# Performance work log

Measured on AMD Instinct MI355X. Metric: run time of the kernel, lower is better.

## Reference

```python
import jax, jax.numpy as jnp
import numpy as np
from jax import lax

IN_FEATURES = 1024
NUM_TAGS = 128
C = NUM_TAGS + 3          # CRF adds start/stop (+1 pad slot per original code)
START_IDX = C - 2
STOP_IDX = C - 1
NEG = -10000.0


def setup_inputs() -> dict:
    key = jax.random.key(0)
    k1, k2, k3, k4 = jax.random.split(key, 4)
    B, L = 64, 512
    x = jax.random.normal(k1, (B, L, IN_FEATURES), dtype=jnp.float32)
    mask = jnp.ones((B, L), dtype=jnp.float32)
    W = jax.random.normal(k2, (C, IN_FEATURES), dtype=jnp.float32) * (1.0 / np.sqrt(IN_FEATURES))
    b = jax.random.normal(k3, (C,), dtype=jnp.float32) * 0.01
    transitions = jax.random.normal(k4, (C, C), dtype=jnp.float32)
    # transitions[i, j] = score of transitioning FROM j TO i
    transitions = transitions.at[START_IDX, :].set(NEG)   # never transition into start
    transitions = transitions.at[:, STOP_IDX].set(NEG)    # never transition out of stop
    return {"x": x, "mask": mask, "W": W, "b": b, "transitions": transitions}


def reference(x, mask, W, b, transitions):
    """CRF forward: linear projection + Viterbi decode.
    Returns (best_score [B], best_paths [B, L])."""
    feats = jnp.einsum("bld,cd->blc", x, W) + b          # [B, L, C]
    B, L, Cn = feats.shape

    init_score = jnp.full((B, Cn), NEG, dtype=feats.dtype).at[:, START_IDX].set(0.0)

    def viterbi_step(score, inp):
        feat_t, mask_t = inp                              # [B, C], [B]
        # acc[b, i, j] = score[b, j] + transitions[i, j]
        acc = score[:, None, :] + transitions[None, :, :]  # [B, C, C]
        best = jnp.max(acc, axis=-1)                      # [B, C]
        bp = jnp.argmax(acc, axis=-1).astype(jnp.int32)   # [B, C]
        m = mask_t[:, None]
        new_score = (best + feat_t) * m + score * (1.0 - m)
        return new_score, bp

    final_score, bps = lax.scan(
        viterbi_step, init_score,
        (jnp.transpose(feats, (1, 0, 2)), mask.T))        # bps: [L, B, C]

    final_score = final_score + transitions[STOP_IDX]     # [B, C]
    best_score = jnp.max(final_score, axis=-1)            # [B]
    best_tag = jnp.argmax(final_score, axis=-1).astype(jnp.int32)  # [B]

    def backtrack(tag, bp_t):
        # tag: current tag at timestep t; bp_t: [B, C] backpointers at t
        prev = jnp.take_along_axis(bp_t, tag[:, None], axis=1)[:, 0]
        return prev, tag                                  # emit tag at timestep t

    _, path = lax.scan(backtrack, best_tag, bps, reverse=True)  # path: [L, B]
    best_paths = path.T                                   # [B, L]
    return best_score, best_paths
```

## Files before the change

### kernel.cpp

```cpp
#include <hip/hip_runtime.h>

#define BB 64
#define LL 512
#define DD 1024
#define CC 131
#define CP 132
#define START_I 129
#define STOP_I 130
#define NEGV -10000.0f

__device__ __forceinline__ void lds_barrier() {
    asm volatile("s_waitcnt lgkmcnt(0)" ::: "memory");
    __builtin_amdgcn_s_barrier();
    __builtin_amdgcn_sched_barrier(0);
}

#define GM 64
#define GK 32
#define LSTR 36

__global__ __launch_bounds__(256, 2) void gemm_feats(
    const float* __restrict__ x, const float* __restrict__ W,
    const float* __restrict__ bias, float* __restrict__ feats)
{
    __shared__ float xs[GM * LSTR];
    __shared__ float ws[CP * LSTR];

    const int tid = threadIdx.x;
    const int m0 = blockIdx.x * GM;
    const int tm = tid & 15;
    const int tj = (tid >> 4) & 15;
    const bool tail = (tj < 3);
    const int tjt = (tj < 3) ? tj : 2;

    float acc[4][8];
    float acct[4];
#pragma unroll
    for (int r = 0; r < 4; ++r) {
        acct[r] = 0.f;
#pragma unroll
        for (int c = 0; c < 8; ++c) acc[r][c] = 0.f;
    }

    for (int kc = 0; kc < DD / GK; ++kc) {
        const int k0 = kc * GK;
        if (kc) __syncthreads();
#pragma unroll
        for (int q = 0; q < 2; ++q) {
            int lin = tid + q * 256;
            int m = lin >> 3, c4 = lin & 7;
            float4 v = *(const float4*)&x[(size_t)(m0 + m) * DD + k0 + c4 * 4];
            *(float4*)&xs[m * LSTR + c4 * 4] = v;
        }
#pragma unroll
        for (int q = 0; q < 5; ++q) {
            int lin = tid + q * 256;
            if (lin < CC * 8) {
                int r = lin >> 3, c4 = lin & 7;
                float4 v = *(const float4*)&W[(size_t)r * DD + k0 + c4 * 4];
                *(float4*)&ws[r * LSTR + c4 * 4] = v;
            }
        }
        __syncthreads();

#pragma unroll
        for (int k4 = 0; k4 < 8; ++k4) {
            float4 xr[4], wr[8], wt;
#pragma unroll
            for (int r = 0; r < 4; ++r)
                xr[r] = *(const float4*)&xs[(tm + 16 * r) * LSTR + k4 * 4];
#pragma unroll
            for (int c = 0; c < 8; ++c)
                wr[c] = *(const float4*)&ws[(tj + 16 * c) * LSTR + k4 * 4];
            wt = *(const float4*)&ws[(128 + tjt) * LSTR + k4 * 4];
#pragma unroll
            for (int r = 0; r < 4; ++r) {
#pragma unroll
                for (int c = 0; c < 8; ++c) {
                    acc[r][c] = fmaf(xr[r].x, wr[c].x, acc[r][c]);
                    acc[r][c] = fmaf(xr[r].y, wr[c].y, acc[r][c]);
                    acc[r][c] = fmaf(xr[r].z, wr[c].z, acc[r][c]);
                    acc[r][c] = fmaf(xr[r].w, wr[c].w, acc[r][c]);
                }
                acct[r] = fmaf(xr[r].x, wt.x, acct[r]);
                acct[r] = fmaf(xr[r].y, wt.y, acct[r]);
                acct[r] = fmaf(xr[r].z, wt.z, acct[r]);
                acct[r] = fmaf(xr[r].w, wt.w, acct[r]);
            }
        }
    }

#pragma unroll
    for (int c = 0; c < 8; ++c) {
        int j = tj + 16 * c;
        float bv = bias[j];
#pragma unroll
        for (int r = 0; r < 4; ++r)
            feats[(size_t)(m0 + tm + 16 * r) * CP + j] = acc[r][c] + bv;
    }
    if (tail) {
        int j = 128 + tj;
        float bv = bias[j];
#pragma unroll
        for (int r = 0; r < 4; ++r)
            feats[(size_t)(m0 + tm + 16 * r) * CP + j] = acct[r] + bv;
    }
}

__global__ __launch_bounds__(576, 1) void viterbi_fwd(
    const float* __restrict__ feats, const float* __restrict__ mask,
    const float* __restrict__ trans, float* __restrict__ hist)
{
    const int b = blockIdx.x;
    const int tid = threadIdx.x;
    const int w = tid >> 6, lane = tid & 63;

    int row, sub;
    bool scw;
    if (w < 8) {
        row = (w >> 2) * 64 + lane;
        sub = w & 3;
        scw = true;
    } else {
        int r = 128 + (lane >> 2);
        row = (r <= 130) ? r : 130;
        sub = lane & 3;
        scw = (lane < 12);
    }

    __shared__ float sbuf[2][160];
    __shared__ float pbuf[4][136];

    float4 T[10];
    {
        const float* tr = trans + (size_t)row * CC;
        const int base = sub * 40;
#pragma unroll
        for (int q = 0; q < 10; ++q) {
            float vx = NEGV, vy = NEGV, vz = NEGV, vw = NEGV;
            int i = base + 4 * q;
            if (i + 0 < CC) vx = tr[i + 0];
            if (i + 1 < CC) vy = tr[i + 1];
            if (i + 2 < CC) vz = tr[i + 2];
            if (i + 3 < CC) vw = tr[i + 3];
            T[q].x = vx; T[q].y = vy; T[q].z = vz; T[q].w = vw;
        }
    }

    for (int q = tid; q < 2 * 160; q += 576) {
        int bi = q / 160, idx = q - bi * 160;
        sbuf[bi][idx] = (bi == 0 && idx == START_I) ? 0.f : NEGV;
    }
    __syncthreads();

    const float* fb = feats + (size_t)b * LL * CP;
    const float* mb = mask + (size_t)b * LL;
    float* hb = hist + (size_t)b * LL * CP;

    const int k = tid;
    const bool cmb = (tid < 131);
    float s_prev = (k == START_I) ? 0.f : NEGV;
    float fv0 = 0.f, fv1 = 0.f, mv0 = 1.f, mv1 = 1.f;
    const float* fb_t = fb + 2 * CP + k;
    const float* mb_t = mb + 2;
    float* hb_k = hb + k;
    if (cmb) { fv0 = fb[k]; fv1 = fb[CP + k]; mv0 = mb[0]; mv1 = mb[1]; }

    for (int t = 0; t < LL; ++t) {
        const int rb = t & 1;

        {
            const float4* s4 = (const float4*)sbuf[rb] + sub * 10;
            float a0 = -3.0e38f, a1 = -3.0e38f, a2 = -3.0e38f, a3 = -3.0e38f;
#pragma unroll
            for (int q = 0; q < 5; ++q) {
                float4 sv = s4[q]; float4 t4 = T[q];
                a0 = fmaxf(fmaxf(sv.x + t4.x, sv.y + t4.y), a0);
                a1 = fmaxf(fmaxf(sv.z + t4.z, sv.w + t4.w), a1);
            }
#pragma unroll
            for (int q = 5; q < 10; ++q) {
                float4 sv = s4[q]; float4 t4 = T[q];
                a2 = fmaxf(fmaxf(sv.x + t4.x, sv.y + t4.y), a2);
                a3 = fmaxf(fmaxf(sv.z + t4.z, sv.w + t4.w), a3);
            }
            if (scw) pbuf[sub][row] = fmaxf(fmaxf(a0, a1), fmaxf(a2, a3));
        }

        lds_barrier();

        if (cmb) {
            float fv2 = 0.f, mv2 = 1.f;
            if (t + 2 < LL) { fv2 = *fb_t; mv2 = *mb_t; }
            fb_t += CP; ++mb_t;

            float p = fmaxf(fmaxf(pbuf[0][k], pbuf[1][k]),
                            fmaxf(pbuf[2][k], pbuf[3][k]));
            float ns = (mv0 != 0.f) ? (p + fv0) : s_prev;
            s_prev = ns;
            sbuf[rb ^ 1][k] = ns;
            *hb_k = ns;
            hb_k += CP;

            fv0 = fv1; fv1 = fv2; mv0 = mv1; mv1 = mv2;
        }

        lds_barrier();
    }
}

__global__ __launch_bounds__(256, 4) void bp_kernel(
    const float* __restrict__ hist, const float* __restrict__ trans,
    unsigned char* __restrict__ bp)
{
    const int b  = blockIdx.x / 5;
    const int jc = blockIdx.x % 5;
    const int tc = blockIdx.y;
    const int tid = threadIdx.x;
    const int j0 = jc * 32;

    __shared__ float Ts[32][136];
    __shared__ float hs[8][132];

    for (int q = 0; q < 17; ++q) {
        int lin = tid + q * 256;
        if (lin < 32 * CC) {
            int r = lin / CC, i = lin - r * CC;
            if (j0 + r < CC) Ts[r][i] = trans[(size_t)(j0 + r) * CC + i];
        }
    }
    {
        const float4* src = (const float4*)(hist + ((size_t)b * LL + tc * 8) * CP);
#pragma unroll
        for (int q = 0; q < 2; ++q) {
            int lin = tid + q * 256;
            if (lin < (8 * CP) / 4) ((float4*)hs)[lin] = src[lin];
        }
    }
    __syncthreads();

    const int jl = tid & 31;
    const int tt = tid >> 5;
    const int j = j0 + jl;
    const int t = tc * 8 + tt + 1;
    if (j >= CC || t >= LL) return;

    float best; int idx;
    {
        float4 tv = *(const float4*)&Ts[jl][128];
        float4 hv = *(const float4*)&hs[tt][128];
        best = hv.z + tv.z; idx = 130;
        float v;
        v = hv.y + tv.y; if (v >= best) { best = v; idx = 129; }
        v = hv.x + tv.x; if (v >= best) { best = v; idx = 128; }
    }
#pragma unroll
    for (int i4 = 31; i4 >= 0; --i4) {
        float4 tv = *(const float4*)&Ts[jl][i4 * 4];
        float4 hv = *(const float4*)&hs[tt][i4 * 4];
        float v;
        v = hv.w + tv.w; if (v >= best) { best = v; idx = i4 * 4 + 3; }
        v = hv.z + tv.z; if (v >= best) { best = v; idx = i4 * 4 + 2; }
        v = hv.y + tv.y; if (v >= best) { best = v; idx = i4 * 4 + 1; }
        v = hv.x + tv.x; if (v >= best) { best = v; idx = i4 * 4 + 0; }
    }
    bp[((size_t)b * LL + t) * CP + j] = (unsigned char)idx;
}

__global__ __launch_bounds__(64, 1) void viterbi_btr(
    const float* __restrict__ hist, const float* __restrict__ trans,
    const unsigned char* __restrict__ bp,
    float* __restrict__ out_score, float* __restrict__ out_path)
{
    const int b = blockIdx.x;
    const int lane = threadIdx.x;
    const float* hb = hist + ((size_t)b * LL + (LL - 1)) * CP;
    const float* ts = trans + (size_t)STOP_I * CC;

    float v0 = hb[lane] + ts[lane];
    float v1 = hb[lane + 64] + ts[lane + 64];
    float v2 = (lane < 3) ? (hb[lane + 128] + ts[lane + 128]) : -3.0e38f;

    float best = v0; int idx = lane;
    if (v1 > best) { best = v1; idx = lane + 64; }
    if (v2 > best) { best = v2; idx = lane + 128; }
#pragma unroll
    for (int off = 32; off >= 1; off >>= 1) {
        float ob = __shfl_xor(best, off, 64);
        int   oi = __shfl_xor(idx, off, 64);
        if (ob > best || (ob == best && oi < idx)) { best = ob; idx = oi; }
    }

    float* op = out_path + (size_t)b * LL;
    if (lane == 0) {
        out_score[b] = best;
        op[LL - 1] = (float)idx;
    }
    int tag = idx;

    __shared__ unsigned char buf[2][1088];
    const unsigned char* bpb = bp + (size_t)b * LL * CP;

    {
        const unsigned int* src = (const unsigned int*)(bpb + (size_t)504 * CP);
        unsigned int* dst = (unsigned int*)buf[1];
#pragma unroll
        for (int q = 0; q < 5; ++q) {
            int lin = lane + q * 64;
            if (lin < 264) dst[lin] = src[lin];
        }
    }
    lds_barrier();

    int cur = 1;
    for (int k = 63; k >= 0; --k) {
        unsigned int r0 = 0, r1 = 0, r2 = 0, r3 = 0, r4 = 0;
        if (k > 0) {
            const unsigned int* src = (const unsigned int*)(bpb + (size_t)(k - 1) * 8 * CP);
            r0 = src[lane];
            r1 = src[lane + 64];
            r2 = src[lane + 128];
            r3 = src[lane + 192];
            if (lane < 8) r4 = src[lane + 256];
        }
        const unsigned char* cb = buf[cur];
#pragma unroll
        for (int s = 7; s >= 0; --s) {
            int t = k * 8 + s;
            if (t >= 1) {
                tag = cb[s * CP + tag];
                if (lane == 0) op[t - 1] = (float)tag;
            }
        }
        if (k > 0) {
            unsigned int* dst = (unsigned int*)buf[cur ^ 1];
            dst[lane] = r0;
            dst[lane + 64] = r1;
            dst[lane + 128] = r2;
            dst[lane + 192] = r3;
            if (lane < 8) dst[lane + 256] = r4;
            lds_barrier();
        }
        cur ^= 1;
    }
}

extern "C" void kernel_launch(void* const* d_in, const int* in_sizes, int n_in,
                              void* d_out, int out_size, void* d_ws, size_t ws_size,
                              hipStream_t stream)
{
    const float* x     = (const float*)d_in[0];
    const float* mask  = (const float*)d_in[1];
    const float* W     = (const float*)d_in[2];
    const float* bias  = (const float*)d_in[3];
    const float* trans = (const float*)d_in[4];

    float* feats = (float*)d_ws;
    float* hist  = feats + (size_t)BB * LL * CP;
    unsigned char* bp = (unsigned char*)(hist + (size_t)BB * LL * CP);
    float* out_score = (float*)d_out;
    float* out_path  = out_score + BB;

    hipLaunchKernelGGL(gemm_feats, dim3((BB * LL) / GM), dim3(256), 0, stream, x, W, bias, feats);
    hipLaunchKernelGGL(viterbi_fwd, dim3(BB), dim3(576), 0, stream, feats, mask, trans, hist);
    hipLaunchKernelGGL(bp_kernel, dim3(BB * 5, 64), dim3(256), 0, stream, hist, trans, bp);
    hipLaunchKernelGGL(viterbi_btr, dim3(BB), dim3(64), 0, stream, hist, trans, bp, out_score, out_path);
}
```

Measured before the change: 682.3 us.

## Repartition Viterbi forward max across 7 column slices with 8 waves

Reworks the work split in the sequential Viterbi forward kernel. Each wave now covers a 20-column slice of the previous scores for two rows (TA/TB), and an eighth wave handles the three extra rows, which drops the block from 9 to 8 waves. The aim is a shorter per-step critical path, with fewer threads meeting at each barrier and fewer shared-memory reads per thread. The cost is 7 partial maxima to combine per step instead of 4, plus more register pressure.

```diff
diff --git a/kernel.cpp b/kernel.cpp
--- a/kernel.cpp
+++ b/kernel.cpp
@@ -107,7 +107,7 @@
     }
 }
 
-__global__ __launch_bounds__(576, 1) void viterbi_fwd(
+__global__ __launch_bounds__(512, 1) void viterbi_fwd(
     const float* __restrict__ feats, const float* __restrict__ mask,
     const float* __restrict__ trans, float* __restrict__ hist)
 {
@@ -115,97 +115,116 @@
     const int tid = threadIdx.x;
     const int w = tid >> 6, lane = tid & 63;
 
-    int row, sub;
-    bool scw;
-    if (w < 8) {
-        row = (w >> 2) * 64 + lane;
-        sub = w & 3;
-        scw = true;
-    } else {
-        int r = 128 + (lane >> 2);
-        row = (r <= 130) ? r : 130;
-        sub = lane & 3;
-        scw = (lane < 12);
-    }
-
-    __shared__ float sbuf[2][160];
-    __shared__ float pbuf[4][136];
-
-    float4 T[10];
-    {
-        const float* tr = trans + (size_t)row * CC;
-        const int base = sub * 40;
-#pragma unroll
-        for (int q = 0; q < 10; ++q) {
-            float vx = NEGV, vy = NEGV, vz = NEGV, vw = NEGV;
-            int i = base + 4 * q;
-            if (i + 0 < CC) vx = tr[i + 0];
-            if (i + 1 < CC) vy = tr[i + 1];
-            if (i + 2 < CC) vz = tr[i + 2];
-            if (i + 3 < CC) vw = tr[i + 3];
-            T[q].x = vx; T[q].y = vy; T[q].z = vz; T[q].w = vw;
-        }
-    }
-
-    for (int q = tid; q < 2 * 160; q += 576) {
-        int bi = q / 160, idx = q - bi * 160;
-        sbuf[bi][idx] = (bi == 0 && idx == START_I) ? 0.f : NEGV;
-    }
-    __syncthreads();
+    __shared__ float sbuf[2][144];
+    __shared__ float pbuf[7][132];
 
     const float* fb = feats + (size_t)b * LL * CP;
     const float* mb = mask + (size_t)b * LL;
     float* hb = hist + (size_t)b * LL * CP;
 
+    int sub, trow = 0;
+    bool twr = false;
+    float4 TA[5], TB[5];
+    if (w < 7) {
+        sub = w;
+        const int i0 = sub * 20;
+        const float* trA = trans + (size_t)lane * CC;
+        const float* trB = trans + (size_t)(64 + lane) * CC;
+#pragma unroll
+        for (int q = 0; q < 5; ++q) {
+            int i = i0 + 4 * q;
+            TA[q].x = (i + 0 < CC) ? trA[i + 0] : NEGV;
+            TA[q].y = (i + 1 < CC) ? trA[i + 1] : NEGV;
+            TA[q].z = (i + 2 < CC) ? trA[i + 2] : NEGV;
+            TA[q].w = (i + 3 < CC) ? trA[i + 3] : NEGV;
+            TB[q].x = (i + 0 < CC) ? trB[i + 0] : NEGV;
+            TB[q].y = (i + 1 < CC) ? trB[i + 1] : NEGV;
+            TB[q].z = (i + 2 < CC) ? trB[i + 2] : NEGV;
+            TB[q].w = (i + 3 < CC) ? trB[i + 3] : NEGV;
+        }
+    } else {
+        const int ln = (lane < 21) ? lane : 20;
+        const int s7 = ln / 3;
+        const int r3 = ln - s7 * 3;
+        sub = s7;
+        trow = 128 + r3;
+        twr = (lane < 21);
+        const int i0 = sub * 20;
+        const float* tr = trans + (size_t)trow * CC;
+#pragma unroll
+        for (int q = 0; q < 5; ++q) {
+            int i = i0 + 4 * q;
+            TA[q].x = (i + 0 < CC) ? tr[i + 0] : NEGV;
+            TA[q].y = (i + 1 < CC) ? tr[i + 1] : NEGV;
+            TA[q].z = (i + 2 < CC) ? tr[i + 2] : NEGV;
+            TA[q].w = (i + 3 < CC) ? tr[i + 3] : NEGV;
+        }
+    }
+
+    for (int q = tid; q < 2 * 144; q += 512) {
+        int bi = q / 144, idx = q - bi * 144;
+        sbuf[bi][idx] = (bi == 0 && idx == START_I) ? 0.f : NEGV;
+    }
+    __syncthreads();
+
     const int k = tid;
-    const bool cmb = (tid < 131);
+    const bool cl = (tid < 131);
     float s_prev = (k == START_I) ? 0.f : NEGV;
     float fv0 = 0.f, fv1 = 0.f, mv0 = 1.f, mv1 = 1.f;
+    if (cl) { fv0 = fb[k]; fv1 = fb[CP + k]; mv0 = mb[0]; mv1 = mb[1]; }
     const float* fb_t = fb + 2 * CP + k;
     const float* mb_t = mb + 2;
-    float* hb_k = hb + k;
-    if (cmb) { fv0 = fb[k]; fv1 = fb[CP + k]; mv0 = mb[0]; mv1 = mb[1]; }
+    float* hb_t = hb + k;
 
     for (int t = 0; t < LL; ++t) {
         const int rb = t & 1;
 
         {
-            const float4* s4 = (const float4*)sbuf[rb] + sub * 10;
-            float a0 = -3.0e38f, a1 = -3.0e38f, a2 = -3.0e38f, a3 = -3.0e38f;
-#pragma unroll
-            for (int q = 0; q < 5; ++q) {
-                float4 sv = s4[q]; float4 t4 = T[q];
-                a0 = fmaxf(fmaxf(sv.x + t4.x, sv.y + t4.y), a0);
-                a1 = fmaxf(fmaxf(sv.z + t4.z, sv.w + t4.w), a1);
+            const float4* s4 = (const float4*)(&sbuf[rb][0]) + sub * 5;
+            if (w < 7) {
+                float a0 = -3.0e38f, a1 = -3.0e38f, b0 = -3.0e38f, b1 = -3.0e38f;
+#pragma unroll
+                for (int q = 0; q < 5; ++q) {
+                    float4 sv = s4[q];
+                    a0 = fmaxf(fmaxf(sv.x + TA[q].x, sv.y + TA[q].y), a0);
+                    a1 = fmaxf(fmaxf(sv.z + TA[q].z, sv.w + TA[q].w), a1);
+                    b0 = fmaxf(fmaxf(sv.x + TB[q].x, sv.y + TB[q].y), b0);
+                    b1 = fmaxf(fmaxf(sv.z + TB[q].z, sv.w + TB[q].w), b1);
+                }
+                pbuf[sub][lane] = fmaxf(a0, a1);
+                pbuf[sub][64 + lane] = fmaxf(b0, b1);
+            } else {
+                float a0 = -3.0e38f, a1 = -3.0e38f;
+#pragma unroll
+                for (int q = 0; q < 5; ++q) {
+                    float4 sv = s4[q];
+                    a0 = fmaxf(fmaxf(sv.x + TA[q].x, sv.y + TA[q].y), a0);
+                    a1 = fmaxf(fmaxf(sv.z + TA[q].z, sv.w + TA[q].w), a1);
+                }
+                if (twr) pbuf[sub][trow] = fmaxf(a0, a1);
             }
-#pragma unroll
-            for (int q = 5; q < 10; ++q) {
-                float4 sv = s4[q]; float4 t4 = T[q];
-                a2 = fmaxf(fmaxf(sv.x + t4.x, sv.y + t4.y), a2);
-                a3 = fmaxf(fmaxf(sv.z + t4.z, sv.w + t4.w), a3);
-            }
-            if (scw) pbuf[sub][row] = fmaxf(fmaxf(a0, a1), fmaxf(a2, a3));
         }
 
         lds_barrier();
 
-        if (cmb) {
-            float fv2 = 0.f, mv2 = 1.f;
-            if (t + 2 < LL) { fv2 = *fb_t; mv2 = *mb_t; }
-            fb_t += CP; ++mb_t;
-
-            float p = fmaxf(fmaxf(pbuf[0][k], pbuf[1][k]),
-                            fmaxf(pbuf[2][k], pbuf[3][k]));
+        float fv2 = 0.f, mv2 = 1.f;
+        if (cl && t + 2 < LL) { fv2 = *fb_t; mv2 = *mb_t; }
+        fb_t += CP; ++mb_t;
+
+        if (cl) {
+            float p = fmaxf(fmaxf(fmaxf(pbuf[0][k], pbuf[1][k]),
+                                  fmaxf(pbuf[2][k], pbuf[3][k])),
+                            fmaxf(fmaxf(pbuf[4][k], pbuf[5][k]), pbuf[6][k]));
             float ns = (mv0 != 0.f) ? (p + fv0) : s_prev;
             s_prev = ns;
             sbuf[rb ^ 1][k] = ns;
-            *hb_k = ns;
-            hb_k += CP;
-
-            fv0 = fv1; fv1 = fv2; mv0 = mv1; mv1 = mv2;
-        }
+            *hb_t = ns;
+        }
+        hb_t += CP;
 
         lds_barrier();
+
+        fv0 = fv1; fv1 = fv2; mv0 = mv1; mv1 = mv2;
     }
 }
 
@@ -362,7 +381,7 @@
     float* out_path  = out_score + BB;
 
     hipLaunchKernelGGL(gemm_feats, dim3((BB * LL) / GM), dim3(256), 0, stream, x, W, bias, feats);
-    hipLaunchKernelGGL(viterbi_fwd, dim3(BB), dim3(576), 0, stream, feats, mask, trans, hist);
+    hipLaunchKernelGGL(viterbi_fwd, dim3(BB), dim3(512), 0, stream, feats, mask, trans, hist);
     hipLaunchKernelGGL(bp_kernel, dim3(BB * 5, 64), dim3(256), 0, stream, hist, trans, bp);
     hipLaunchKernelGGL(viterbi_btr, dim3(BB), dim3(64), 0, stream, hist, trans, bp, out_score, out_path);
 }
```

Result: faster. 595.1 us (-12.8%).
